# Kernel optimization log

Hardware: AMD Instinct MI355X
Metric: run time of the kernel (lower is better)

The kernel has to match this reference:

```python
import jax, jax.numpy as jnp
import numpy as np

# Dimensions per init_kwargs
B, S, D = 2, 2048, 1024          # batch, seq, hidden_size
F = 4096                          # intermediate_size
E, K = 8, 2                       # moe_num_experts, moe_top_k
EPS = 1e-9


def setup_inputs() -> dict:
    key = jax.random.key(0)
    k1, k2, k3, k4 = jax.random.split(key, 4)
    x = jax.random.normal(k1, (B, S, D), dtype=jnp.float32)
    # gate: Linear(D, E, bias=False) -> stored as [D, E] for x @ w_gate
    w_gate = jax.random.normal(k2, (D, E), dtype=jnp.float32) * 0.02
    # per-expert gate_up_proj: Linear(D, 2F, bias=False), stacked over experts -> [E, D, 2F]
    w_gate_up = jax.random.normal(k3, (E, D, 2 * F), dtype=jnp.float32) * 0.02
    # per-expert down_proj: Linear(F, D, bias=False), stacked -> [E, F, D]
    w_down = jax.random.normal(k4, (E, F, D), dtype=jnp.float32) * 0.02
    return {"x": x, "w_gate": w_gate, "w_gate_up": w_gate_up, "w_down": w_down}


def reference(x, w_gate, w_gate_up, w_down):
    # Router
    gate_logits = x @ w_gate                       # [B,S,E]
    gate_probs = jax.nn.softmax(gate_logits, axis=-1)
    # top-k masking + renormalization (top_k < num_experts)
    topk_vals, topk_idx = jax.lax.top_k(gate_probs, K)           # [B,S,K]
    masked = jnp.sum(jax.nn.one_hot(topk_idx, E, dtype=gate_probs.dtype)
                     * topk_vals[..., None], axis=-2)            # [B,S,E]
    denom = jnp.maximum(jnp.sum(masked, axis=-1, keepdims=True), EPS)
    gate_probs = masked / denom

    # Dense per-expert SwiGLU FFN on all tokens (faithful to reference impl)
    gu = jnp.einsum('bsd,edh->ebsh', x, w_gate_up)               # [E,B,S,2F]
    g, u = jnp.split(gu, 2, axis=-1)                             # [E,B,S,F] each
    act = jax.nn.silu(g) * u                                     # [E,B,S,F]
    expert_out = jnp.einsum('ebsf,efd->ebsd', act, w_down)       # [E,B,S,D]

    # Gate-weighted combine
    return jnp.einsum('bse,ebsd->bsd', gate_probs, expert_out)   # [B,S,D]
```

## Files before the change

### kernel.cpp

```cpp
#include <hip/hip_runtime.h>
#include <stdint.h>

#define NTOK 4096
#define DMODEL 1024
#define FF 4096
#define NEXP 8

typedef __bf16 bf16x8 __attribute__((ext_vector_type(8)));
typedef float f32x4 __attribute__((ext_vector_type(4)));

__device__ __forceinline__ unsigned short f2bf(float f) {
  union { float f; unsigned u; } v; v.f = f;
  unsigned r = v.u + 0x7fffu + ((v.u >> 16) & 1u);
  return (unsigned short)(r >> 16);
}

__global__ __launch_bounds__(256) void k_convert_x(const float4* __restrict__ in,
                                                   ushort4* __restrict__ out, int n4) {
  int stride = gridDim.x * blockDim.x;
  for (int i = blockIdx.x * blockDim.x + threadIdx.x; i < n4; i += stride) {
    float4 v = in[i];
    out[i] = make_ushort4(f2bf(v.x), f2bf(v.y), f2bf(v.z), f2bf(v.w));
  }
}

__global__ __launch_bounds__(256) void k_transpose_bf16(const float* __restrict__ in,
                                                        unsigned short* __restrict__ out,
                                                        int R, int C) {
  __shared__ float tile[64][65];
  const size_t slab = (size_t)R * C;
  const float* ip = in + slab * blockIdx.z;
  unsigned short* op = out + slab * blockIdx.z;
  int c0 = blockIdx.x * 64, r0 = blockIdx.y * 64;
  int tx = threadIdx.x & 15, ty = threadIdx.x >> 4;
#pragma unroll
  for (int i = 0; i < 4; ++i) {
    int r = ty + 16 * i;
    float4 v = *(const float4*)(ip + (size_t)(r0 + r) * C + c0 + tx * 4);
    tile[r][tx * 4 + 0] = v.x;
    tile[r][tx * 4 + 1] = v.y;
    tile[r][tx * 4 + 2] = v.z;
    tile[r][tx * 4 + 3] = v.w;
  }
  __syncthreads();
#pragma unroll
  for (int i = 0; i < 4; ++i) {
    int q = ty + 16 * i;
    ushort4 o = make_ushort4(f2bf(tile[tx * 4 + 0][q]), f2bf(tile[tx * 4 + 1][q]),
                             f2bf(tile[tx * 4 + 2][q]), f2bf(tile[tx * 4 + 3][q]));
    *(ushort4*)(op + (size_t)(c0 + q) * R + r0 + tx * 4) = o;
  }
}

__global__ __launch_bounds__(256) void k_router(const float* __restrict__ x,
                                                const float* __restrict__ wg,
                                                int* __restrict__ cnt,
                                                int* __restrict__ elist,
                                                float* __restrict__ gw) {
  int wave = threadIdx.x >> 6, lane = threadIdx.x & 63;
  int t = blockIdx.x * 4 + wave;
  const float* xp = x + (size_t)t * DMODEL;
  float a[8] = {0, 0, 0, 0, 0, 0, 0, 0};
#pragma unroll
  for (int i = 0; i < DMODEL / 64; ++i) {
    int d = lane + 64 * i;
    float xv = xp[d];
    float4 w0 = *(const float4*)(wg + d * 8);
    float4 w1 = *(const float4*)(wg + d * 8 + 4);
    a[0] += xv * w0.x; a[1] += xv * w0.y; a[2] += xv * w0.z; a[3] += xv * w0.w;
    a[4] += xv * w1.x; a[5] += xv * w1.y; a[6] += xv * w1.z; a[7] += xv * w1.w;
  }
#pragma unroll
  for (int off = 32; off > 0; off >>= 1)
#pragma unroll
    for (int e = 0; e < 8; ++e) a[e] += __shfl_down(a[e], off, 64);
  if (lane == 0) {
    int e0 = 0;
    for (int e = 1; e < 8; ++e) if (a[e] > a[e0]) e0 = e;
    int e1 = (e0 == 0) ? 1 : 0;
    for (int e = 0; e < 8; ++e) if (e != e0 && a[e] > a[e1]) e1 = e;
    float p = __expf(a[e1] - a[e0]);
    float inv = 1.0f / (1.0f + p);
    int p0 = atomicAdd(&cnt[e0], 1);
    elist[e0 * NTOK + p0] = 2 * t;
    gw[2 * t] = inv;
    int p1 = atomicAdd(&cnt[e1], 1);
    elist[e1 * NTOK + p1] = 2 * t + 1;
    gw[2 * t + 1] = p * inv;
  }
}

__global__ __launch_bounds__(256) void k_gemm1(const unsigned short* __restrict__ xb,
                                               const unsigned short* __restrict__ wgu,
                                               const int* __restrict__ cnt,
                                               const int* __restrict__ elist,
                                               unsigned short* __restrict__ act)
{
  __shared__ __align__(16) unsigned short sA[128 * 64];
  __shared__ __align__(16) unsigned short sB[128 * 64];

  const int e = blockIdx.z;
  const int n_e = cnt[e];
  const int m0 = blockIdx.y * 128;
  if (m0 >= n_e) return;
  const int c0 = blockIdx.x * 64;
  const int tid = threadIdx.x;
  const int w = tid >> 6, lane = tid & 63;
  const int wr = w >> 1, wc = w & 1;
  const int* el = elist + e * NTOK;
  const int csub = (((lane & 7) ^ (lane >> 3)) * 8);

  int tokrow[4];
  size_t baddr[4];
  const unsigned short* wb = wgu + (size_t)e * (2 * FF) * DMODEL;
#pragma unroll
  for (int i = 0; i < 4; ++i) {
    int r = w * 32 + i * 8 + (lane >> 3);
    int idx = m0 + r;
    tokrow[i] = el[idx < n_e ? idx : 0] >> 1;
    int half = r >> 6, off = r & 63;
    int gr = (off < 32) ? (c0 + half * 32 + off) : (FF + c0 + half * 32 + (off - 32));
    baddr[i] = (size_t)gr * DMODEL;
  }

  f32x4 acc[4][4];
  f32x4 zero = {0.f, 0.f, 0.f, 0.f};
#pragma unroll
  for (int m = 0; m < 4; ++m)
#pragma unroll
    for (int n = 0; n < 4; ++n) acc[m][n] = zero;

  for (int k0 = 0; k0 < DMODEL; k0 += 64) {
    __syncthreads();
#pragma unroll
    for (int i = 0; i < 4; ++i) {
      const unsigned short* g = xb + (size_t)tokrow[i] * DMODEL + k0 + csub;
      __builtin_amdgcn_global_load_lds((const __attribute__((address_space(1))) void*)g,
                                       (__attribute__((address_space(3))) void*)(sA + (w * 4 + i) * 512),
                                       16, 0, 0);
    }
#pragma unroll
    for (int i = 0; i < 4; ++i) {
      const unsigned short* g = wb + baddr[i] + k0 + csub;
      __builtin_amdgcn_global_load_lds((const __attribute__((address_space(1))) void*)g,
                                       (__attribute__((address_space(3))) void*)(sB + (w * 4 + i) * 512),
                                       16, 0, 0);
    }
    __syncthreads();
#pragma unroll
    for (int kk = 0; kk < 2; ++kk) {
      const int xk = ((kk * 4 + (lane >> 4)) ^ (lane & 7)) * 8;
      bf16x8 af[4], bfr[4];
#pragma unroll
      for (int m = 0; m < 4; ++m)
        af[m] = *(const bf16x8*)(sA + (wr * 64 + m * 16 + (lane & 15)) * 64 + xk);
#pragma unroll
      for (int n = 0; n < 4; ++n)
        bfr[n] = *(const bf16x8*)(sB + (wc * 64 + n * 16 + (lane & 15)) * 64 + xk);
#pragma unroll
      for (int m = 0; m < 4; ++m)
#pragma unroll
        for (int n = 0; n < 4; ++n)
          acc[m][n] = __builtin_amdgcn_mfma_f32_16x16x32_bf16(af[m], bfr[n], acc[m][n], 0, 0, 0);
    }
  }

#pragma unroll
  for (int m = 0; m < 4; ++m) {
#pragma unroll
    for (int r = 0; r < 4; ++r) {
      int idx = m0 + wr * 64 + m * 16 + (lane >> 4) * 4 + r;
      if (idx < n_e) {
        int p = el[idx];
        unsigned short* ap = act + (size_t)p * FF + c0 + wc * 32;
#pragma unroll
        for (int n = 0; n < 2; ++n) {
          float g = acc[m][n][r];
          float u = acc[m][n + 2][r];
          float s = g / (1.0f + __expf(-g));
          ap[n * 16 + (lane & 15)] = f2bf(s * u);
        }
      }
    }
  }
}

__global__ __launch_bounds__(256) void k_gemm2(const unsigned short* __restrict__ actb,
                                               const unsigned short* __restrict__ wd,
                                               const int* __restrict__ cnt,
                                               const int* __restrict__ elist,
                                               const float* __restrict__ gw,
                                               float* __restrict__ out_slot)
{
  __shared__ __align__(16) unsigned short sA[128 * 64];
  __shared__ __align__(16) unsigned short sB[128 * 64];

  const int e = blockIdx.z;
  const int n_e = cnt[e];
  const int m0 = blockIdx.y * 128;
  if (m0 >= n_e) return;
  const int n0 = blockIdx.x * 128;
  const int tid = threadIdx.x;
  const int w = tid >> 6, lane = tid & 63;
  const int wr = w >> 1, wc = w & 1;
  const int* el = elist + e * NTOK;
  const int csub = (((lane & 7) ^ (lane >> 3)) * 8);

  int prow[4];
  size_t baddr[4];
  const unsigned short* wb = wd + (size_t)e * DMODEL * FF;
#pragma unroll
  for (int i = 0; i < 4; ++i) {
    int r = w * 32 + i * 8 + (lane >> 3);
    int idx = m0 + r;
    prow[i] = el[idx < n_e ? idx : 0];
    baddr[i] = (size_t)(n0 + r) * FF;
  }

  f32x4 acc[4][4];
  f32x4 zero = {0.f, 0.f, 0.f, 0.f};
#pragma unroll
  for (int m = 0; m < 4; ++m)
#pragma unroll
    for (int n = 0; n < 4; ++n) acc[m][n] = zero;

  for (int k0 = 0; k0 < FF; k0 += 64) {
    __syncthreads();
#pragma unroll
    for (int i = 0; i < 4; ++i) {
      const unsigned short* g = actb + (size_t)prow[i] * FF + k0 + csub;
      __builtin_amdgcn_global_load_lds((const __attribute__((address_space(1))) void*)g,
                                       (__attribute__((address_space(3))) void*)(sA + (w * 4 + i) * 512),
                                       16, 0, 0);
    }
#pragma unroll
    for (int i = 0; i < 4; ++i) {
      const unsigned short* g = wb + baddr[i] + k0 + csub;
      __builtin_amdgcn_global_load_lds((const __attribute__((address_space(1))) void*)g,
                                       (__attribute__((address_space(3))) void*)(sB + (w * 4 + i) * 512),
                                       16, 0, 0);
    }
    __syncthreads();
#pragma unroll
    for (int kk = 0; kk < 2; ++kk) {
      const int xk = ((kk * 4 + (lane >> 4)) ^ (lane & 7)) * 8;
      bf16x8 af[4], bfr[4];
#pragma unroll
      for (int m = 0; m < 4; ++m)
        af[m] = *(const bf16x8*)(sA + (wr * 64 + m * 16 + (lane & 15)) * 64 + xk);
#pragma unroll
      for (int n = 0; n < 4; ++n)
        bfr[n] = *(const bf16x8*)(sB + (wc * 64 + n * 16 + (lane & 15)) * 64 + xk);
#pragma unroll
      for (int m = 0; m < 4; ++m)
#pragma unroll
        for (int n = 0; n < 4; ++n)
          acc[m][n] = __builtin_amdgcn_mfma_f32_16x16x32_bf16(af[m], bfr[n], acc[m][n], 0, 0, 0);
    }
  }

#pragma unroll
  for (int m = 0; m < 4; ++m) {
#pragma unroll
    for (int r = 0; r < 4; ++r) {
      int idx = m0 + wr * 64 + m * 16 + (lane >> 4) * 4 + r;
      if (idx < n_e) {
        int p = el[idx];
        float wgt = gw[p];
        float* op = out_slot + (size_t)p * DMODEL + n0 + wc * 64;
#pragma unroll
        for (int n = 0; n < 4; ++n)
          op[n * 16 + (lane & 15)] = acc[m][n][r] * wgt;
      }
    }
  }
}

__global__ __launch_bounds__(256) void k_combine(const float4* __restrict__ slot,
                                                 float4* __restrict__ out, int n4) {
  int stride = gridDim.x * blockDim.x;
  for (int i = blockIdx.x * blockDim.x + threadIdx.x; i < n4; i += stride) {
    int t = i >> 8;
    int j = i & 255;
    float4 a = slot[(size_t)(2 * t) * 256 + j];
    float4 b = slot[(size_t)(2 * t + 1) * 256 + j];
    float4 o;
    o.x = a.x + b.x; o.y = a.y + b.y; o.z = a.z + b.z; o.w = a.w + b.w;
    out[i] = o;
  }
}

extern "C" void kernel_launch(void* const* d_in, const int* in_sizes, int n_in,
                              void* d_out, int out_size, void* d_ws, size_t ws_size,
                              hipStream_t stream) {
  const float* x   = (const float*)d_in[0];
  const float* wg  = (const float*)d_in[1];
  const float* wgu = (const float*)d_in[2];
  const float* wd  = (const float*)d_in[3];
  float* out = (float*)d_out;

  char* ws = (char*)d_ws;
  size_t off = 0;
  auto alloc = [&](size_t bytes) -> char* {
    char* p = ws + off;
    off += (bytes + 255) & ~(size_t)255;
    return p;
  };
  unsigned short* wgu_t = (unsigned short*)alloc((size_t)NEXP * 2 * FF * DMODEL * 2);
  unsigned short* wd_t  = (unsigned short*)alloc((size_t)NEXP * DMODEL * FF * 2);
  unsigned short* actb  = (unsigned short*)alloc((size_t)2 * NTOK * FF * 2);
  float* out_slot       = (float*)alloc((size_t)2 * NTOK * DMODEL * 4);
  unsigned short* xb    = (unsigned short*)alloc((size_t)NTOK * DMODEL * 2);
  int* elist            = (int*)alloc((size_t)NEXP * NTOK * 4);
  float* gw             = (float*)alloc((size_t)2 * NTOK * 4);
  int* cnt              = (int*)alloc(256);
  if (off > ws_size) return;

  hipMemsetAsync(cnt, 0, 256, stream);
  k_convert_x<<<1024, 256, 0, stream>>>((const float4*)x, (ushort4*)xb, NTOK * DMODEL / 4);
  k_transpose_bf16<<<dim3(2 * FF / 64, DMODEL / 64, NEXP), 256, 0, stream>>>(wgu, wgu_t, DMODEL, 2 * FF);
  k_transpose_bf16<<<dim3(DMODEL / 64, FF / 64, NEXP), 256, 0, stream>>>(wd, wd_t, FF, DMODEL);
  k_router<<<NTOK / 4, 256, 0, stream>>>(x, wg, cnt, elist, gw);
  k_gemm1<<<dim3(FF / 64, NTOK / 128, NEXP), 256, 0, stream>>>(xb, wgu_t, cnt, elist, actb);
  k_gemm2<<<dim3(DMODEL / 128, NTOK / 128, NEXP), 256, 0, stream>>>(actb, wd_t, cnt, elist, gw, out_slot);
  k_combine<<<2048, 256, 0, stream>>>((const float4*)out_slot, (float4*)out, NTOK * DMODEL / 4);
}
```

Before: 648.6 us.

## Enlarge expert GEMM tiles to 256 rows with 512 threads and double-buffered LDS

Both grouped expert GEMMs move from 128-row tiles with 256 threads to 256-row tiles with 8 waves. gemm1 also widens its column tile to 128. The LDS staging is now double-buffered, so the next k-slice's global-to-LDS loads are issued before computing the current one, and there is one barrier per iteration instead of two. This is meant to improve weight reuse per loaded tile and overlap memory latency with MFMA work, at the cost of much more LDS (64KB in gemm1) and more accumulator registers, which may limit occupancy. It also wastes more work on partially filled tiles when an expert's token count is not a multiple of 256.

Result: no change. 640.5 us (-1.3%).

```diff
diff --git a/kernel.cpp b/kernel.cpp
--- a/kernel.cpp
+++ b/kernel.cpp
@@ -90,86 +90,98 @@
   }
 }
 
-__global__ __launch_bounds__(256) void k_gemm1(const unsigned short* __restrict__ xb,
-                                               const unsigned short* __restrict__ wgu,
-                                               const int* __restrict__ cnt,
-                                               const int* __restrict__ elist,
-                                               unsigned short* __restrict__ act)
+__global__ __launch_bounds__(512, 2) void k_gemm1(const unsigned short* __restrict__ xb,
+                                                  const unsigned short* __restrict__ wgu,
+                                                  const int* __restrict__ cnt,
+                                                  const int* __restrict__ elist,
+                                                  unsigned short* __restrict__ act)
 {
-  __shared__ __align__(16) unsigned short sA[128 * 64];
-  __shared__ __align__(16) unsigned short sB[128 * 64];
+  __shared__ __align__(16) unsigned short sA[2][256 * 64];
+  __shared__ __align__(16) unsigned short sB[2][256 * 64];
 
   const int e = blockIdx.z;
   const int n_e = cnt[e];
-  const int m0 = blockIdx.y * 128;
+  const int m0 = blockIdx.y * 256;
   if (m0 >= n_e) return;
-  const int c0 = blockIdx.x * 64;
+  const int c0 = blockIdx.x * 128;
   const int tid = threadIdx.x;
   const int w = tid >> 6, lane = tid & 63;
-  const int wr = w >> 1, wc = w & 1;
+  const int wr = w >> 2, wc = w & 3;
   const int* el = elist + e * NTOK;
-  const int csub = (((lane & 7) ^ (lane >> 3)) * 8);
+  const int csub = ((lane & 7) ^ (lane >> 3)) * 8;
+  const int srow = w * 8 + (lane >> 3);
 
   int tokrow[4];
   size_t baddr[4];
   const unsigned short* wb = wgu + (size_t)e * (2 * FF) * DMODEL;
 #pragma unroll
   for (int i = 0; i < 4; ++i) {
-    int r = w * 32 + i * 8 + (lane >> 3);
+    int r = i * 64 + srow;
     int idx = m0 + r;
     tokrow[i] = el[idx < n_e ? idx : 0] >> 1;
-    int half = r >> 6, off = r & 63;
-    int gr = (off < 32) ? (c0 + half * 32 + off) : (FF + c0 + half * 32 + (off - 32));
-    baddr[i] = (size_t)gr * DMODEL;
-  }
-
-  f32x4 acc[4][4];
+    int strip = r >> 6, off = r & 63;
+    int wrow = (off < 32) ? (c0 + strip * 32 + off) : (FF + c0 + strip * 32 + off - 32);
+    baddr[i] = (size_t)wrow * DMODEL;
+  }
+
+  f32x4 acc[8][4];
   f32x4 zero = {0.f, 0.f, 0.f, 0.f};
 #pragma unroll
-  for (int m = 0; m < 4; ++m)
+  for (int m = 0; m < 8; ++m)
 #pragma unroll
     for (int n = 0; n < 4; ++n) acc[m][n] = zero;
 
-  for (int k0 = 0; k0 < DMODEL; k0 += 64) {
-    __syncthreads();
+  auto stage = [&](int buf, int k0) {
 #pragma unroll
     for (int i = 0; i < 4; ++i) {
       const unsigned short* g = xb + (size_t)tokrow[i] * DMODEL + k0 + csub;
       __builtin_amdgcn_global_load_lds((const __attribute__((address_space(1))) void*)g,
-                                       (__attribute__((address_space(3))) void*)(sA + (w * 4 + i) * 512),
+                                       (__attribute__((address_space(3))) void*)(&sA[buf][(i * 64 + w * 8) * 64]),
                                        16, 0, 0);
     }
 #pragma unroll
     for (int i = 0; i < 4; ++i) {
       const unsigned short* g = wb + baddr[i] + k0 + csub;
       __builtin_amdgcn_global_load_lds((const __attribute__((address_space(1))) void*)g,
-                                       (__attribute__((address_space(3))) void*)(sB + (w * 4 + i) * 512),
+                                       (__attribute__((address_space(3))) void*)(&sB[buf][(i * 64 + w * 8) * 64]),
                                        16, 0, 0);
     }
-    __syncthreads();
+  };
+
+  auto compute = [&](int buf) {
 #pragma unroll
     for (int kk = 0; kk < 2; ++kk) {
       const int xk = ((kk * 4 + (lane >> 4)) ^ (lane & 7)) * 8;
-      bf16x8 af[4], bfr[4];
-#pragma unroll
-      for (int m = 0; m < 4; ++m)
-        af[m] = *(const bf16x8*)(sA + (wr * 64 + m * 16 + (lane & 15)) * 64 + xk);
+      bf16x8 af[8], bf[4];
+#pragma unroll
+      for (int m = 0; m < 8; ++m)
+        af[m] = *(const bf16x8*)(&sA[buf][(wr * 128 + m * 16 + (lane & 15)) * 64 + xk]);
 #pragma unroll
       for (int n = 0; n < 4; ++n)
-        bfr[n] = *(const bf16x8*)(sB + (wc * 64 + n * 16 + (lane & 15)) * 64 + xk);
-#pragma unroll
-      for (int m = 0; m < 4; ++m)
+        bf[n] = *(const bf16x8*)(&sB[buf][(wc * 64 + n * 16 + (lane & 15)) * 64 + xk]);
+#pragma unroll
+      for (int m = 0; m < 8; ++m)
 #pragma unroll
         for (int n = 0; n < 4; ++n)
-          acc[m][n] = __builtin_amdgcn_mfma_f32_16x16x32_bf16(af[m], bfr[n], acc[m][n], 0, 0, 0);
-    }
-  }
-
-#pragma unroll
-  for (int m = 0; m < 4; ++m) {
+          acc[m][n] = __builtin_amdgcn_mfma_f32_16x16x32_bf16(af[m], bf[n], acc[m][n], 0, 0, 0);
+    }
+  };
+
+  stage(0, 0);
+  __syncthreads();
+  int cur = 0;
+  for (int t = 0; t < DMODEL / 64; ++t) {
+    if (t + 1 < DMODEL / 64) stage(cur ^ 1, (t + 1) * 64);
+    compute(cur);
+    __syncthreads();
+    cur ^= 1;
+  }
+
+#pragma unroll
+  for (int m = 0; m < 8; ++m) {
 #pragma unroll
     for (int r = 0; r < 4; ++r) {
-      int idx = m0 + wr * 64 + m * 16 + (lane >> 4) * 4 + r;
+      int idx = m0 + wr * 128 + m * 16 + (lane >> 4) * 4 + r;
       if (idx < n_e) {
         int p = el[idx];
         unsigned short* ap = act + (size_t)p * FF + c0 + wc * 32;
@@ -185,91 +197,104 @@
   }
 }
 
-__global__ __launch_bounds__(256) void k_gemm2(const unsigned short* __restrict__ actb,
-                                               const unsigned short* __restrict__ wd,
-                                               const int* __restrict__ cnt,
-                                               const int* __restrict__ elist,
-                                               const float* __restrict__ gw,
-                                               float* __restrict__ out_slot)
+__global__ __launch_bounds__(512, 2) void k_gemm2(const unsigned short* __restrict__ actb,
+                                                  const unsigned short* __restrict__ wd,
+                                                  const int* __restrict__ cnt,
+                                                  const int* __restrict__ elist,
+                                                  const float* __restrict__ gw,
+                                                  float* __restrict__ out_slot)
 {
-  __shared__ __align__(16) unsigned short sA[128 * 64];
-  __shared__ __align__(16) unsigned short sB[128 * 64];
+  __shared__ __align__(16) unsigned short sA[2][256 * 64];
+  __shared__ __align__(16) unsigned short sB[2][128 * 64];
 
   const int e = blockIdx.z;
   const int n_e = cnt[e];
-  const int m0 = blockIdx.y * 128;
+  const int m0 = blockIdx.y * 256;
   if (m0 >= n_e) return;
   const int n0 = blockIdx.x * 128;
   const int tid = threadIdx.x;
   const int w = tid >> 6, lane = tid & 63;
-  const int wr = w >> 1, wc = w & 1;
+  const int wr = w >> 2, wc = w & 3;
   const int* el = elist + e * NTOK;
-  const int csub = (((lane & 7) ^ (lane >> 3)) * 8);
+  const int csub = ((lane & 7) ^ (lane >> 3)) * 8;
+  const int srow = w * 8 + (lane >> 3);
 
   int prow[4];
-  size_t baddr[4];
+  size_t baddr[2];
   const unsigned short* wb = wd + (size_t)e * DMODEL * FF;
 #pragma unroll
   for (int i = 0; i < 4; ++i) {
-    int r = w * 32 + i * 8 + (lane >> 3);
-    int idx = m0 + r;
+    int idx = m0 + i * 64 + srow;
     prow[i] = el[idx < n_e ? idx : 0];
-    baddr[i] = (size_t)(n0 + r) * FF;
-  }
-
-  f32x4 acc[4][4];
+  }
+#pragma unroll
+  for (int i = 0; i < 2; ++i)
+    baddr[i] = (size_t)(n0 + i * 64 + srow) * FF;
+
+  f32x4 acc[8][2];
   f32x4 zero = {0.f, 0.f, 0.f, 0.f};
 #pragma unroll
-  for (int m = 0; m < 4; ++m)
-#pragma unroll
-    for (int n = 0; n < 4; ++n) acc[m][n] = zero;
-
-  for (int k0 = 0; k0 < FF; k0 += 64) {
-    __syncthreads();
+  for (int m = 0; m < 8; ++m)
+#pragma unroll
+    for (int n = 0; n < 2; ++n) acc[m][n] = zero;
+
+  auto stage = [&](int buf, int k0) {
 #pragma unroll
     for (int i = 0; i < 4; ++i) {
       const unsigned short* g = actb + (size_t)prow[i] * FF + k0 + csub;
       __builtin_amdgcn_global_load_lds((const __attribute__((address_space(1))) void*)g,
-                                       (__attribute__((address_space(3))) void*)(sA + (w * 4 + i) * 512),
+                                       (__attribute__((address_space(3))) void*)(&sA[buf][(i * 64 + w * 8) * 64]),
                                        16, 0, 0);
     }
 #pragma unroll
-    for (int i = 0; i < 4; ++i) {
+    for (int i = 0; i < 2; ++i) {
       const unsigned short* g = wb + baddr[i] + k0 + csub;
       __builtin_amdgcn_global_load_lds((const __attribute__((address_space(1))) void*)g,
-                                       (__attribute__((address_space(3))) void*)(sB + (w * 4 + i) * 512),
+                                       (__attribute__((address_space(3))) void*)(&sB[buf][(i * 64 + w * 8) * 64]),
                                        16, 0, 0);
     }
-    __syncthreads();
+  };
+
+  auto compute = [&](int buf) {
 #pragma unroll
     for (int kk = 0; kk < 2; ++kk) {
       const int xk = ((kk * 4 + (lane >> 4)) ^ (lane & 7)) * 8;
-      bf16x8 af[4], bfr[4];
-#pragma unroll
-      for (int m = 0; m < 4; ++m)
-        af[m] = *(const bf16x8*)(sA + (wr * 64 + m * 16 + (lane & 15)) * 64 + xk);
-#pragma unroll
-      for (int n = 0; n < 4; ++n)
-        bfr[n] = *(const bf16x8*)(sB + (wc * 64 + n * 16 + (lane & 15)) * 64 + xk);
-#pragma unroll
-      for (int m = 0; m < 4; ++m)
-#pragma unroll
-        for (int n = 0; n < 4; ++n)
-          acc[m][n] = __builtin_amdgcn_mfma_f32_16x16x32_bf16(af[m], bfr[n], acc[m][n], 0, 0, 0);
-    }
-  }
-
-#pragma unroll
-  for (int m = 0; m < 4; ++m) {
+      bf16x8 af[8], bf[2];
+#pragma unroll
+      for (int m = 0; m < 8; ++m)
+        af[m] = *(const bf16x8*)(&sA[buf][(wr * 128 + m * 16 + (lane & 15)) * 64 + xk]);
+#pragma unroll
+      for (int n = 0; n < 2; ++n)
+        bf[n] = *(const bf16x8*)(&sB[buf][(wc * 32 + n * 16 + (lane & 15)) * 64 + xk]);
+#pragma unroll
+      for (int m = 0; m < 8; ++m)
+#pragma unroll
+        for (int n = 0; n < 2; ++n)
+          acc[m][n] = __builtin_amdgcn_mfma_f32_16x16x32_bf16(af[m], bf[n], acc[m][n], 0, 0, 0);
+    }
+  };
+
+  stage(0, 0);
+  __syncthreads();
+  int cur = 0;
+  for (int t = 0; t < FF / 64; ++t) {
+    if (t + 1 < FF / 64) stage(cur ^ 1, (t + 1) * 64);
+    compute(cur);
+    __syncthreads();
+    cur ^= 1;
+  }
+
+#pragma unroll
+  for (int m = 0; m < 8; ++m) {
 #pragma unroll
     for (int r = 0; r < 4; ++r) {
-      int idx = m0 + wr * 64 + m * 16 + (lane >> 4) * 4 + r;
+      int idx = m0 + wr * 128 + m * 16 + (lane >> 4) * 4 + r;
       if (idx < n_e) {
         int p = el[idx];
         float wgt = gw[p];
-        float* op = out_slot + (size_t)p * DMODEL + n0 + wc * 64;
-#pragma unroll
-        for (int n = 0; n < 4; ++n)
+        float* op = out_slot + (size_t)p * DMODEL + n0 + wc * 32;
+#pragma unroll
+        for (int n = 0; n < 2; ++n)
           op[n * 16 + (lane & 15)] = acc[m][n][r] * wgt;
       }
     }
@@ -321,7 +346,7 @@
   k_transpose_bf16<<<dim3(2 * FF / 64, DMODEL / 64, NEXP), 256, 0, stream>>>(wgu, wgu_t, DMODEL, 2 * FF);
   k_transpose_bf16<<<dim3(DMODEL / 64, FF / 64, NEXP), 256, 0, stream>>>(wd, wd_t, FF, DMODEL);
   k_router<<<NTOK / 4, 256, 0, stream>>>(x, wg, cnt, elist, gw);
-  k_gemm1<<<dim3(FF / 64, NTOK / 128, NEXP), 256, 0, stream>>>(xb, wgu_t, cnt, elist, actb);
-  k_gemm2<<<dim3(DMODEL / 128, NTOK / 128, NEXP), 256, 0, stream>>>(actb, wd_t, cnt, elist, gw, out_slot);
+  k_gemm1<<<dim3(FF / 128, NTOK / 256, NEXP), 512, 0, stream>>>(xb, wgu_t, cnt, elist, actb);
+  k_gemm2<<<dim3(DMODEL / 128, NTOK / 256, NEXP), 512, 0, stream>>>(actb, wd_t, cnt, elist, gw, out_slot);
   k_combine<<<2048, 256, 0, stream>>>((const float4*)out_slot, (float4*)out, NTOK * DMODEL / 4);
 }
```
